# Kernel optimization log

Measured on AMD Instinct MI355X. Metric: run time of the kernel, lower is better.

Reference implementation:

```python
import jax, jax.numpy as jnp
import numpy as np

B, T, N, P = 4, 512, 160, 32
DT2_DX2 = 0.16  # (dt/dx)^2, chosen CFL-stable for c in [1, 1.5]


def setup_inputs() -> dict:
    key = jax.random.key(0)
    k1, k2, k3, k4, k5 = jax.random.split(key, 5)
    x = 0.1 * jax.random.normal(k1, (B, T), dtype=jnp.float32)          # source waveform per batch
    c = 1.0 + 0.5 * jax.random.uniform(k2, (N, N), dtype=jnp.float32)   # wave speed field
    rho = 1.0 + 0.5 * jax.random.uniform(k3, (N, N), dtype=jnp.float32) # density field
    probe_i = jax.random.randint(k4, (P,), 0, N)
    probe_j = jax.random.randint(k5, (P,), 0, N)
    return {
        "x": x, "c": c, "rho": rho,
        "src_i": 80, "src_j": 80,
        "probe_i": probe_i, "probe_j": probe_j,
    }


def _laplacian(h):
    # 5-point stencil with zero-Dirichlet boundaries; h: [B, N, N]
    hp = jnp.pad(h, ((0, 0), (1, 1), (1, 1)))
    return (hp[:, 2:, 1:-1] + hp[:, :-2, 1:-1]
            + hp[:, 1:-1, 2:] + hp[:, 1:-1, :-2] - 4.0 * h)


def reference(x, c, rho, src_i, src_j, probe_i, probe_j):
    coeff = (DT2_DX2 * c * c / rho).astype(x.dtype)  # [N, N]

    def step(carry, xi):
        h1, h2 = carry
        hn = 2.0 * h1 - h2 + coeff * _laplacian(h1)   # leapfrog cell update
        hn = hn.at[:, src_i, src_j].add(xi)           # source injection, xi: [B]
        y = hn[:, probe_i, probe_j]                   # probe readout -> [B, P]
        return (hn, h1), y

    h0 = jnp.zeros((x.shape[0], c.shape[0], c.shape[1]), dtype=x.dtype)
    (_, _), ys = jax.lax.scan(step, (h0, h0), x.T)    # ys: [T, B, P]
    return jnp.transpose(ys, (1, 0, 2))               # [B, T, P]
```

## Files before the change

kernel.cpp:

```cpp
#include <hip/hip_runtime.h>


#define NB   4
#define NBK  4
#define OWN  40
#define D_EX 20
#define NT   512
#define NN   160
#define NP   32
#define C_DT 0.16f

#define TGX   32
#define TPR   16
#define NTHR  (TPR*TGX)
#define EROWS (2*TPR + 2)
#define K_ENT 6

#define SLAB      (D_EX*NN)
#define GB_FLOATS (NB*NBK*2*2*SLAB)
#define FLAG_OFF  (GB_FLOATS*4)

typedef float f4 __attribute__((ext_vector_type(4)));

#if defined(__has_builtin)
#if __has_builtin(__builtin_amdgcn_update_dpp)
#define HAVE_DPP 1
#endif
#endif

__device__ __forceinline__ float shr1(float v) {
#ifdef HAVE_DPP
    return __int_as_float(__builtin_amdgcn_update_dpp(
        0, __float_as_int(v), 0x138 , 0xf, 0xf, true));
#else
    return __shfl_up(v, 1, 64);
#endif
}
__device__ __forceinline__ float shl1(float v) {
#ifdef HAVE_DPP
    return __int_as_float(__builtin_amdgcn_update_dpp(
        0, __float_as_int(v), 0x130 , 0xf, 0xf, true));
#else
    return __shfl_down(v, 1, 64);
#endif
}

__global__ __launch_bounds__(NTHR, 1) void wave_kernel(
    const float* __restrict__ x,
    const float* __restrict__ cmat,
    const float* __restrict__ rho,
    const int*   __restrict__ src_i_p,
    const int*   __restrict__ src_j_p,
    const int*   __restrict__ probe_i,
    const int*   __restrict__ probe_j,
    float*       __restrict__ y,
    float*       __restrict__ gw,
    int*         __restrict__ flags)
{
    __shared__ f4    eb4[2][EROWS][TGX];
    __shared__ float eb1[2][EROWS][TGX];
    __shared__ float xbuf[NT];
    __shared__ int   pco[2*NP];

    const int bid   = blockIdx.x;
    const int batch = bid & 7;
    if (batch >= NB) return;
    const int blk   = bid >> 3;

    const int own_s = blk * OWN;
    const int own_e = own_s + OWN;
    const int ext_s = (own_s - D_EX < 0)  ? 0  : own_s - D_EX;
    const int ext_e = (own_e + D_EX > NN) ? NN : own_e + D_EX;
    const int npr   = (ext_e - ext_s) / 5;

    const int tid = threadIdx.x;
    const int pr  = tid >> 5;
    const int cg  = tid & 31;
    const bool act = pr < npr;
    const int gr0 = ext_s + 5*pr;
    const int c0  = 5*cg;

    {
        float* e4 = (float*)&eb4[0][0][0];
        for (int i = tid; i < 2*EROWS*TGX*4; i += NTHR) e4[i] = 0.0f;
        float* e1 = &eb1[0][0][0];
        for (int i = tid; i < 2*EROWS*TGX; i += NTHR) e1[i] = 0.0f;
        for (int i = tid; i < NT; i += NTHR) xbuf[i] = x[batch*NT + i];
        if (tid < NP) { pco[tid] = probe_i[tid]; pco[NP + tid] = probe_j[tid]; }
    }

    const int si = src_i_p[0];
    const int sj = src_j_p[0];

    float hA[5][5], hB[5][5], cf[5][5], c2[5][5];
    #pragma unroll
    for (int i = 0; i < 5; ++i)
        #pragma unroll
        for (int j = 0; j < 5; ++j) {
            float cfv = 0.0f;
            if (act) {
                const float cc = cmat[(gr0+i)*NN + (c0+j)];
                const float rr = rho[(gr0+i)*NN + (c0+j)];
                cfv = C_DT * cc * cc / rr;
            }
            cf[i][j] = cfv;
            c2[i][j] = 2.0f - 4.0f * cfv;
            hA[i][j] = 0.0f;
            hB[i][j] = 0.0f;
        }

    unsigned srcMask = 0;
    if (act && gr0 <= si && si < gr0 + 5 && c0 <= sj && sj < c0 + 5)
        srcMask = 1u << ((si - gr0)*5 + (sj - c0));

    __syncthreads();

    unsigned long long ent = 0;
    int ecnt = 0;
    if (act && gr0 >= own_s && gr0 < own_e) {
        for (int p = 0; p < NP; ++p) {
            const int r = pco[p], c = pco[NP + p];
            if (r >= gr0 && r < gr0 + 5 && c >= c0 && c < c0 + 5) {
                const int ij = (r - gr0)*5 + (c - c0);
                if (ecnt < K_ENT)
                    ent |= ((unsigned long long)(unsigned)(p | (ij << 5))) << (10*ecnt);
                ecnt++;
            }
        }
    }

    const int bid2 = batch*NBK + blk;
    float* sTop = nullptr; float* sBot = nullptr;
    const float* rTop = nullptr; const float* rBot = nullptr;
    if (blk > 0 && gr0 >= own_s && gr0 < own_s + D_EX)
        sTop = gw + (size_t)(bid2*2 + 0)*2*SLAB + (gr0 - own_s)*NN + c0;
    if (blk < NBK-1 && gr0 >= own_e - D_EX && gr0 < own_e)
        sBot = gw + (size_t)(bid2*2 + 1)*2*SLAB + (gr0 - (own_e - D_EX))*NN + c0;
    if (blk > 0 && act && gr0 < own_s)
        rTop = gw + (size_t)((bid2-1)*2 + 1)*2*SLAB + (gr0 - (own_s - D_EX))*NN + c0;
    if (blk < NBK-1 && act && gr0 >= own_e)
        rBot = gw + (size_t)((bid2+1)*2 + 0)*2*SLAB + (gr0 - own_e)*NN + c0;
    int* const flagSelf = &flags[bid2];
    int* const flagUp   = &flags[bid2 - 1];
    int* const flagDn   = &flags[bid2 + 1];

    float* const yb = y + (size_t)batch*NT*NP;

#define STEP(HS, HD, TT, PIN, POUT)                                           \
    {                                                                         \
        const int tt = (TT);                                                  \
        const f4    nh4 = eb4[PIN][2*pr    ][cg];                             \
        const float nhe = eb1[PIN][2*pr    ][cg];                             \
        const f4    sh4 = eb4[PIN][2*pr + 3][cg];                             \
        const float she = eb1[PIN][2*pr + 3][cg];                             \
        const float nh[5] = { nh4[0], nh4[1], nh4[2], nh4[3], nhe };          \
        const float sh[5] = { sh4[0], sh4[1], sh4[2], sh4[3], she };          \
        float wh[5], eh[5];                                                   \
        _Pragma("unroll")                                                     \
        for (int i = 0; i < 5; ++i) {                                         \
            const float tw = shr1(HS[i][4]);                                  \
            wh[i] = (cg == 0) ? 0.0f : tw;                                    \
            const float te = shl1(HS[i][0]);                                  \
            eh[i] = (cg == TGX-1) ? 0.0f : te;                                \
        }                                                                     \
        _Pragma("unroll")                                                     \
        for (int i = 0; i < 5; ++i) {                                         \
            _Pragma("unroll")                                                 \
            for (int j = 0; j < 5; ++j) {                                     \
                const float up = (i == 0) ? nh[j] : HS[i-1][j];               \
                const float dn = (i == 4) ? sh[j] : HS[i+1][j];               \
                const float lf = (j == 0) ? wh[i] : HS[i][j-1];               \
                const float rt = (j == 4) ? eh[i] : HS[i][j+1];               \
                const float s  = (up + dn) + (lf + rt);                       \
                const float t1 = __builtin_fmaf(c2[i][j], HS[i][j], -HD[i][j]); \
                HD[i][j] = __builtin_fmaf(cf[i][j], s, t1);                   \
            }                                                                 \
        }                                                                     \
        if (srcMask) {                                                        \
            const float xt = xbuf[tt];                                        \
            _Pragma("unroll")                                                 \
            for (int i = 0; i < 5; ++i)                                       \
                _Pragma("unroll")                                             \
                for (int j = 0; j < 5; ++j)                                   \
                    if (srcMask & (1u << (i*5 + j))) HD[i][j] += xt;          \
        }                                                                     \
        eb4[POUT][2*pr + 1][cg] = (f4){ HD[0][0], HD[0][1], HD[0][2], HD[0][3] }; \
        eb1[POUT][2*pr + 1][cg] = HD[0][4];                                   \
        eb4[POUT][2*pr + 2][cg] = (f4){ HD[4][0], HD[4][1], HD[4][2], HD[4][3] }; \
        eb1[POUT][2*pr + 2][cg] = HD[4][4];                                   \
        if (ecnt) {                                                           \
            float* const yt = yb + (size_t)tt * NP;                           \
            _Pragma("unroll")                                                 \
            for (int k = 0; k < K_ENT; ++k) {                                 \
                if (k < ecnt) {                                               \
                    const int e  = (int)((ent >> (10*k)) & 0x3FF);            \
                    const int p  = e & 31;                                    \
                    const int ij = e >> 5;                                    \
                    float v = 0.0f;                                           \
                    _Pragma("unroll")                                         \
                    for (int i = 0; i < 5; ++i)                               \
                        _Pragma("unroll")                                     \
                        for (int j = 0; j < 5; ++j)                           \
                            if (ij == i*5 + j) v = HD[i][j];                  \
                    yt[p] = v;                                                \
                }                                                             \
            }                                                                 \
        }                                                                     \
        __syncthreads();                                                      \
    }

    int t = 0, g = 0;
    while (t < NT) {
        const int steps = (NT - t < D_EX) ? (NT - t) : D_EX;
        for (int k = 0; k < steps; k += 2) {
            STEP(hA, hB, t + k,     0, 1);
            STEP(hB, hA, t + k + 1, 1, 0);
        }
        t += steps;
        if (t >= NT) break;

        if (sTop) {
            #pragma unroll
            for (int i = 0; i < 5; ++i) {
                *(f4*)(sTop + i*NN) = (f4){ hA[i][0], hA[i][1], hA[i][2], hA[i][3] };
                sTop[i*NN + 4] = hA[i][4];
                *(f4*)(sTop + SLAB + i*NN) = (f4){ hB[i][0], hB[i][1], hB[i][2], hB[i][3] };
                sTop[SLAB + i*NN + 4] = hB[i][4];
            }
        }
        if (sBot) {
            #pragma unroll
            for (int i = 0; i < 5; ++i) {
                *(f4*)(sBot + i*NN) = (f4){ hA[i][0], hA[i][1], hA[i][2], hA[i][3] };
                sBot[i*NN + 4] = hA[i][4];
                *(f4*)(sBot + SLAB + i*NN) = (f4){ hB[i][0], hB[i][1], hB[i][2], hB[i][3] };
                sBot[SLAB + i*NN + 4] = hB[i][4];
            }
        }
        __threadfence();
        __syncthreads();
        if (tid == 0) {
            __hip_atomic_fetch_add(flagSelf, 1, __ATOMIC_RELEASE, __HIP_MEMORY_SCOPE_AGENT);
            if (blk > 0)
                while (__hip_atomic_load(flagUp, __ATOMIC_ACQUIRE, __HIP_MEMORY_SCOPE_AGENT) < g + 1) {}
            if (blk < NBK-1)
                while (__hip_atomic_load(flagDn, __ATOMIC_ACQUIRE, __HIP_MEMORY_SCOPE_AGENT) < g + 1) {}
        }
        __syncthreads();
        {
            const float* rp = rTop ? rTop : rBot;
            if (rp) {
                #pragma unroll
                for (int i = 0; i < 5; ++i) {
                    const f4 v1 = *(const f4*)(rp + i*NN);
                    hA[i][0] = v1[0]; hA[i][1] = v1[1]; hA[i][2] = v1[2]; hA[i][3] = v1[3];
                    hA[i][4] = rp[i*NN + 4];
                    const f4 v2 = *(const f4*)(rp + SLAB + i*NN);
                    hB[i][0] = v2[0]; hB[i][1] = v2[1]; hB[i][2] = v2[2]; hB[i][3] = v2[3];
                    hB[i][4] = rp[SLAB + i*NN + 4];
                }
                eb4[0][2*pr + 1][cg] = (f4){ hA[0][0], hA[0][1], hA[0][2], hA[0][3] };
                eb1[0][2*pr + 1][cg] = hA[0][4];
                eb4[0][2*pr + 2][cg] = (f4){ hA[4][0], hA[4][1], hA[4][2], hA[4][3] };
                eb1[0][2*pr + 2][cg] = hA[4][4];
            }
        }
        __syncthreads();
        g++;
    }
#undef STEP
}

extern "C" void kernel_launch(void* const* d_in, const int* in_sizes, int n_in,
                              void* d_out, int out_size, void* d_ws, size_t ws_size,
                              hipStream_t stream) {
    const float* x    = (const float*)d_in[0];
    const float* cmat = (const float*)d_in[1];
    const float* rho  = (const float*)d_in[2];
    const int*   si   = (const int*)d_in[3];
    const int*   sj   = (const int*)d_in[4];
    const int*   pi   = (const int*)d_in[5];
    const int*   pj   = (const int*)d_in[6];
    float*       yout = (float*)d_out;
    float*       gbuf = (float*)d_ws;
    int*         flg  = (int*)((char*)d_ws + FLAG_OFF);

    hipMemsetAsync(flg, 0, NB*NBK*sizeof(int), stream);

    wave_kernel<<<NB*8, NTHR, 0, stream>>>(x, cmat, rho, si, sj, pi, pj,
                                           yout, gbuf, flg);
}
```

Baseline: 644.6 us.

## Exchange intra-wave halo rows via cross-half shuffles, halve LDS halo traffic

Pairs of 32-thread row groups that share a 64-lane wavefront now exchange their adjacent boundary rows with a cross-half shuffle instead of going through LDS. Only the halo rows crossing wavefront boundaries are written to and read from shared memory, which roughly halves the per-step LDS stores and loads and shrinks the halo buffer. The cost is extra shuffle instructions and select logic that depends on row parity, plus more complex edge handling.

Result: slower. 692.6 us (+7.4%).

```diff
diff --git a/kernel.cpp b/kernel.cpp
--- a/kernel.cpp
+++ b/kernel.cpp
@@ -10,11 +10,11 @@
 #define NP   32
 #define C_DT 0.16f
 
-#define TGX   32
-#define TPR   16
-#define NTHR  (TPR*TGX)
-#define EROWS (2*TPR + 2)
-#define K_ENT 6
+#define TGX    32
+#define TPR    16
+#define NTHR   (TPR*TGX)
+#define ESLOTS (TPR + 2)
+#define K_ENT  6
 
 #define SLAB      (D_EX*NN)
 #define GB_FLOATS (NB*NBK*2*2*SLAB)
@@ -57,8 +57,8 @@
     float*       __restrict__ gw,
     int*         __restrict__ flags)
 {
-    __shared__ f4    eb4[2][EROWS][TGX];
-    __shared__ float eb1[2][EROWS][TGX];
+    __shared__ f4    eb4[2][ESLOTS][TGX];
+    __shared__ float eb1[2][ESLOTS][TGX];
     __shared__ float xbuf[NT];
     __shared__ int   pco[2*NP];
 
@@ -76,15 +76,16 @@
     const int tid = threadIdx.x;
     const int pr  = tid >> 5;
     const int cg  = tid & 31;
+    const int oddr = pr & 1;
     const bool act = pr < npr;
     const int gr0 = ext_s + 5*pr;
     const int c0  = 5*cg;
 
     {
         float* e4 = (float*)&eb4[0][0][0];
-        for (int i = tid; i < 2*EROWS*TGX*4; i += NTHR) e4[i] = 0.0f;
+        for (int i = tid; i < 2*ESLOTS*TGX*4; i += NTHR) e4[i] = 0.0f;
         float* e1 = &eb1[0][0][0];
-        for (int i = tid; i < 2*EROWS*TGX; i += NTHR) e1[i] = 0.0f;
+        for (int i = tid; i < 2*ESLOTS*TGX; i += NTHR) e1[i] = 0.0f;
         for (int i = tid; i < NT; i += NTHR) xbuf[i] = x[batch*NT + i];
         if (tid < NP) { pco[tid] = probe_i[tid]; pco[NP + tid] = probe_j[tid]; }
     }
@@ -146,15 +147,27 @@
 
     float* const yb = y + (size_t)batch*NT*NP;
 
+    const int rdSlot = oddr ? (pr + 2) : pr;
+    const int wrSlot = pr + 1;
+    f4*    const rd4a = &eb4[0][rdSlot][cg]; f4*    const rd4b = &eb4[1][rdSlot][cg];
+    float* const rd1a = &eb1[0][rdSlot][cg]; float* const rd1b = &eb1[1][rdSlot][cg];
+    f4*    const wr4a = &eb4[0][wrSlot][cg]; f4*    const wr4b = &eb4[1][wrSlot][cg];
+    float* const wr1a = &eb1[0][wrSlot][cg]; float* const wr1b = &eb1[1][wrSlot][cg];
+
 #define STEP(HS, HD, TT, PIN, POUT)                                           \
     {                                                                         \
         const int tt = (TT);                                                  \
-        const f4    nh4 = eb4[PIN][2*pr    ][cg];                             \
-        const float nhe = eb1[PIN][2*pr    ][cg];                             \
-        const f4    sh4 = eb4[PIN][2*pr + 3][cg];                             \
-        const float she = eb1[PIN][2*pr + 3][cg];                             \
-        const float nh[5] = { nh4[0], nh4[1], nh4[2], nh4[3], nhe };          \
-        const float sh[5] = { sh4[0], sh4[1], sh4[2], sh4[3], she };          \
+          \
+        const f4    l4 = *(PIN ? rd4b : rd4a);                                \
+        const float l1 = *(PIN ? rd1b : rd1a);                                \
+            \
+        float rcv[5];                                                         \
+        _Pragma("unroll")                                                     \
+        for (int j = 0; j < 5; ++j) {                                         \
+            const float snd = oddr ? HS[0][j] : HS[4][j];                     \
+            rcv[j] = __shfl_xor(snd, 32, 64);                                 \
+        }                                                                     \
+                                                    \
         float wh[5], eh[5];                                                   \
         _Pragma("unroll")                                                     \
         for (int i = 0; i < 5; ++i) {                                         \
@@ -163,17 +176,37 @@
             const float te = shl1(HS[i][0]);                                  \
             eh[i] = (cg == TGX-1) ? 0.0f : te;                                \
         }                                                                     \
+           \
         _Pragma("unroll")                                                     \
-        for (int i = 0; i < 5; ++i) {                                         \
+        for (int i = 1; i < 4; ++i) {                                         \
             _Pragma("unroll")                                                 \
             for (int j = 0; j < 5; ++j) {                                     \
-                const float up = (i == 0) ? nh[j] : HS[i-1][j];               \
-                const float dn = (i == 4) ? sh[j] : HS[i+1][j];               \
                 const float lf = (j == 0) ? wh[i] : HS[i][j-1];               \
                 const float rt = (j == 4) ? eh[i] : HS[i][j+1];               \
-                const float s  = (up + dn) + (lf + rt);                       \
+                const float s  = (HS[i-1][j] + HS[i+1][j]) + (lf + rt);       \
                 const float t1 = __builtin_fmaf(c2[i][j], HS[i][j], -HD[i][j]); \
                 HD[i][j] = __builtin_fmaf(cf[i][j], s, t1);                   \
+            }                                                                 \
+        }                                                                     \
+                                   \
+        _Pragma("unroll")                                                     \
+        for (int j = 0; j < 5; ++j) {                                         \
+            const float lv = (j==0)?l4[0]:(j==1)?l4[1]:(j==2)?l4[2]:(j==3)?l4[3]:l1; \
+            const float nh = oddr ? rcv[j] : lv;                              \
+            const float sh = oddr ? lv : rcv[j];                              \
+            {                                                                 \
+                const float lf = (j == 0) ? wh[0] : HS[0][j-1];               \
+                const float rt = (j == 4) ? eh[0] : HS[0][j+1];               \
+                const float s  = (nh + HS[1][j]) + (lf + rt);                 \
+                const float t1 = __builtin_fmaf(c2[0][j], HS[0][j], -HD[0][j]); \
+                HD[0][j] = __builtin_fmaf(cf[0][j], s, t1);                   \
+            }                                                                 \
+            {                                                                 \
+                const float lf = (j == 0) ? wh[4] : HS[4][j-1];               \
+                const float rt = (j == 4) ? eh[4] : HS[4][j+1];               \
+                const float s  = (HS[3][j] + sh) + (lf + rt);                 \
+                const float t1 = __builtin_fmaf(c2[4][j], HS[4][j], -HD[4][j]); \
+                HD[4][j] = __builtin_fmaf(cf[4][j], s, t1);                   \
             }                                                                 \
         }                                                                     \
         if (srcMask) {                                                        \
@@ -184,16 +217,21 @@
                 for (int j = 0; j < 5; ++j)                                   \
                     if (srcMask & (1u << (i*5 + j))) HD[i][j] += xt;          \
         }                                                                     \
-        eb4[POUT][2*pr + 1][cg] = (f4){ HD[0][0], HD[0][1], HD[0][2], HD[0][3] }; \
-        eb1[POUT][2*pr + 1][cg] = HD[0][4];                                   \
-        eb4[POUT][2*pr + 2][cg] = (f4){ HD[4][0], HD[4][1], HD[4][2], HD[4][3] }; \
-        eb1[POUT][2*pr + 2][cg] = HD[4][4];                                   \
+            \
+        {                                                                     \
+            const f4 ev = (f4){ oddr ? HD[4][0] : HD[0][0],                   \
+                                oddr ? HD[4][1] : HD[0][1],                   \
+                                oddr ? HD[4][2] : HD[0][2],                   \
+                                oddr ? HD[4][3] : HD[0][3] };                 \
+            *(POUT ? wr4b : wr4a) = ev;                                       \
+            *(POUT ? wr1b : wr1a) = oddr ? HD[4][4] : HD[0][4];               \
+        }                                                                     \
         if (ecnt) {                                                           \
             float* const yt = yb + (size_t)tt * NP;                           \
             _Pragma("unroll")                                                 \
-            for (int k = 0; k < K_ENT; ++k) {                                 \
-                if (k < ecnt) {                                               \
-                    const int e  = (int)((ent >> (10*k)) & 0x3FF);            \
+            for (int k2 = 0; k2 < K_ENT; ++k2) {                              \
+                if (k2 < ecnt) {                                              \
+                    const int e  = (int)((ent >> (10*k2)) & 0x3FF);           \
                     const int p  = e & 31;                                    \
                     const int ij = e >> 5;                                    \
                     float v = 0.0f;                                           \
@@ -259,10 +297,12 @@
                     hB[i][0] = v2[0]; hB[i][1] = v2[1]; hB[i][2] = v2[2]; hB[i][3] = v2[3];
                     hB[i][4] = rp[SLAB + i*NN + 4];
                 }
-                eb4[0][2*pr + 1][cg] = (f4){ hA[0][0], hA[0][1], hA[0][2], hA[0][3] };
-                eb1[0][2*pr + 1][cg] = hA[0][4];
-                eb4[0][2*pr + 2][cg] = (f4){ hA[4][0], hA[4][1], hA[4][2], hA[4][3] };
-                eb1[0][2*pr + 2][cg] = hA[4][4];
+                const f4 rv = (f4){ oddr ? hA[4][0] : hA[0][0],
+                                    oddr ? hA[4][1] : hA[0][1],
+                                    oddr ? hA[4][2] : hA[0][2],
+                                    oddr ? hA[4][3] : hA[0][3] };
+                *wr4a = rv;
+                *wr1a = oddr ? hA[4][4] : hA[0][4];
             }
         }
         __syncthreads();
```

## Fuse two leapfrog steps per barrier using a two-deep halo with redundant compute

Applied to the files above, without the earlier changes.

Each thread now advances two time steps per round. It computes an intermediate 7x7 field over its 5x5 tile plus a one-cell halo, using two-row halos exchanged through a reorganised shared-memory buffer. This halves the number of block-wide barriers and LDS exchanges per time step. In exchange it adds redundant stencil work on halo cells, needs more registers for the extended coefficient array and window, and uses a larger shared-memory footprint.

Measured after the change: 915.9 us. +42.1%, slower.

```diff
diff --git a/kernel.cpp b/kernel.cpp
--- a/kernel.cpp
+++ b/kernel.cpp
@@ -13,7 +13,7 @@
 #define TGX   32
 #define TPR   16
 #define NTHR  (TPR*TGX)
-#define EROWS (2*TPR + 2)
+#define NSLOT (TPR + 2)
 #define K_ENT 6
 
 #define SLAB      (D_EX*NN)
@@ -45,6 +45,18 @@
 #endif
 }
 
+#define BROW9(dst, v0,v1,v2,v3,v4) {                                          \
+    dst[2]=(v0); dst[3]=(v1); dst[4]=(v2); dst[5]=(v3); dst[6]=(v4);          \
+    const float _m2 = shr1((v3)), _m1 = shr1((v4));                           \
+    const float _p5 = shl1((v0)), _p6 = shl1((v1));                           \
+    dst[0]=(cg==0)?0.0f:_m2;      dst[1]=(cg==0)?0.0f:_m1;                    \
+    dst[7]=(cg==TGX-1)?0.0f:_p5;  dst[8]=(cg==TGX-1)?0.0f:_p6; }
+
+#define BROW7(dst, v0,v1,v2,v3,v4) {                                          \
+    dst[1]=(v0); dst[2]=(v1); dst[3]=(v2); dst[4]=(v3); dst[5]=(v4);          \
+    const float _m1 = shr1((v4)); const float _p5 = shl1((v0));               \
+    dst[0]=(cg==0)?0.0f:_m1;      dst[6]=(cg==TGX-1)?0.0f:_p5; }
+
 __global__ __launch_bounds__(NTHR, 1) void wave_kernel(
     const float* __restrict__ x,
     const float* __restrict__ cmat,
@@ -57,8 +69,8 @@
     float*       __restrict__ gw,
     int*         __restrict__ flags)
 {
-    __shared__ f4    eb4[2][EROWS][TGX];
-    __shared__ float eb1[2][EROWS][TGX];
+    __shared__ f4    L4[2][6][NSLOT][TGX];
+    __shared__ float L1[2][6][NSLOT][TGX];
     __shared__ float xbuf[NT];
     __shared__ int   pco[2*NP];
 
@@ -81,10 +93,10 @@
     const int c0  = 5*cg;
 
     {
-        float* e4 = (float*)&eb4[0][0][0];
-        for (int i = tid; i < 2*EROWS*TGX*4; i += NTHR) e4[i] = 0.0f;
-        float* e1 = &eb1[0][0][0];
-        for (int i = tid; i < 2*EROWS*TGX; i += NTHR) e1[i] = 0.0f;
+        float* z4 = (float*)&L4[0][0][0][0];
+        for (int i = tid; i < 2*6*NSLOT*TGX*4; i += NTHR) z4[i] = 0.0f;
+        float* z1 = &L1[0][0][0][0];
+        for (int i = tid; i < 2*6*NSLOT*TGX; i += NTHR) z1[i] = 0.0f;
         for (int i = tid; i < NT; i += NTHR) xbuf[i] = x[batch*NT + i];
         if (tid < NP) { pco[tid] = probe_i[tid]; pco[NP + tid] = probe_j[tid]; }
     }
@@ -92,26 +104,35 @@
     const int si = src_i_p[0];
     const int sj = src_j_p[0];
 
-    float hA[5][5], hB[5][5], cf[5][5], c2[5][5];
+    float hA[5][5], hB[5][5], cfx[7][7];
+    #pragma unroll
+    for (int ii = -1; ii <= 5; ++ii)
+        #pragma unroll
+        for (int jj = -1; jj <= 5; ++jj) {
+            float cfv = 0.0f;
+            const int r = gr0 + ii, c = c0 + jj;
+            if (act && r >= 0 && r < NN && c >= 0 && c < NN) {
+                const float cc = cmat[r*NN + c];
+                const float rr = rho[r*NN + c];
+                cfv = C_DT * cc * cc / rr;
+            }
+            cfx[ii+1][jj+1] = cfv;
+        }
     #pragma unroll
     for (int i = 0; i < 5; ++i)
         #pragma unroll
-        for (int j = 0; j < 5; ++j) {
-            float cfv = 0.0f;
-            if (act) {
-                const float cc = cmat[(gr0+i)*NN + (c0+j)];
-                const float rr = rho[(gr0+i)*NN + (c0+j)];
-                cfv = C_DT * cc * cc / rr;
-            }
-            cf[i][j] = cfv;
-            c2[i][j] = 2.0f - 4.0f * cfv;
-            hA[i][j] = 0.0f;
-            hB[i][j] = 0.0f;
-        }
+        for (int j = 0; j < 5; ++j) { hA[i][j] = 0.0f; hB[i][j] = 0.0f; }
 
     unsigned srcMask = 0;
     if (act && gr0 <= si && si < gr0 + 5 && c0 <= sj && sj < c0 + 5)
         srcMask = 1u << ((si - gr0)*5 + (sj - c0));
+    unsigned long long srcW = 0ull;
+    if (act) {
+        for (int ii = -1; ii <= 5; ++ii)
+            for (int jj = -1; jj <= 5; ++jj)
+                if (gr0 + ii == si && c0 + jj == sj)
+                    srcW |= 1ull << ((ii+1)*7 + (jj+1));
+    }
 
     __syncthreads();
 
@@ -146,75 +167,107 @@
 
     float* const yb = y + (size_t)batch*NT*NP;
 
-#define STEP(HS, HD, TT, PIN, POUT)                                           \
-    {                                                                         \
-        const int tt = (TT);                                                  \
-        const f4    nh4 = eb4[PIN][2*pr    ][cg];                             \
-        const float nhe = eb1[PIN][2*pr    ][cg];                             \
-        const f4    sh4 = eb4[PIN][2*pr + 3][cg];                             \
-        const float she = eb1[PIN][2*pr + 3][cg];                             \
-        const float nh[5] = { nh4[0], nh4[1], nh4[2], nh4[3], nhe };          \
-        const float sh[5] = { sh4[0], sh4[1], sh4[2], sh4[3], she };          \
-        float wh[5], eh[5];                                                   \
-        _Pragma("unroll")                                                     \
-        for (int i = 0; i < 5; ++i) {                                         \
-            const float tw = shr1(HS[i][4]);                                  \
-            wh[i] = (cg == 0) ? 0.0f : tw;                                    \
-            const float te = shl1(HS[i][0]);                                  \
-            eh[i] = (cg == TGX-1) ? 0.0f : te;                                \
-        }                                                                     \
-        _Pragma("unroll")                                                     \
-        for (int i = 0; i < 5; ++i) {                                         \
-            _Pragma("unroll")                                                 \
-            for (int j = 0; j < 5; ++j) {                                     \
-                const float up = (i == 0) ? nh[j] : HS[i-1][j];               \
-                const float dn = (i == 4) ? sh[j] : HS[i+1][j];               \
-                const float lf = (j == 0) ? wh[i] : HS[i][j-1];               \
-                const float rt = (j == 4) ? eh[i] : HS[i][j+1];               \
-                const float s  = (up + dn) + (lf + rt);                       \
-                const float t1 = __builtin_fmaf(c2[i][j], HS[i][j], -HD[i][j]); \
-                HD[i][j] = __builtin_fmaf(cf[i][j], s, t1);                   \
-            }                                                                 \
-        }                                                                     \
-        if (srcMask) {                                                        \
-            const float xt = xbuf[tt];                                        \
-            _Pragma("unroll")                                                 \
-            for (int i = 0; i < 5; ++i)                                       \
-                _Pragma("unroll")                                             \
-                for (int j = 0; j < 5; ++j)                                   \
-                    if (srcMask & (1u << (i*5 + j))) HD[i][j] += xt;          \
-        }                                                                     \
-        eb4[POUT][2*pr + 1][cg] = (f4){ HD[0][0], HD[0][1], HD[0][2], HD[0][3] }; \
-        eb1[POUT][2*pr + 1][cg] = HD[0][4];                                   \
-        eb4[POUT][2*pr + 2][cg] = (f4){ HD[4][0], HD[4][1], HD[4][2], HD[4][3] }; \
-        eb1[POUT][2*pr + 2][cg] = HD[4][4];                                   \
-        if (ecnt) {                                                           \
-            float* const yt = yb + (size_t)tt * NP;                           \
-            _Pragma("unroll")                                                 \
-            for (int k = 0; k < K_ENT; ++k) {                                 \
-                if (k < ecnt) {                                               \
-                    const int e  = (int)((ent >> (10*k)) & 0x3FF);            \
-                    const int p  = e & 31;                                    \
-                    const int ij = e >> 5;                                    \
-                    float v = 0.0f;                                           \
-                    _Pragma("unroll")                                         \
-                    for (int i = 0; i < 5; ++i)                               \
-                        _Pragma("unroll")                                     \
-                        for (int j = 0; j < 5; ++j)                           \
-                            if (ij == i*5 + j) v = HD[i][j];                  \
-                    yt[p] = v;                                                \
-                }                                                             \
-            }                                                                 \
-        }                                                                     \
-        __syncthreads();                                                      \
-    }
+#define PUBLISH(P) {                                                           \
+    L4[P][0][pr+1][cg]=(f4){hA[0][0],hA[0][1],hA[0][2],hA[0][3]}; L1[P][0][pr+1][cg]=hA[0][4]; \
+    L4[P][1][pr+1][cg]=(f4){hA[1][0],hA[1][1],hA[1][2],hA[1][3]}; L1[P][1][pr+1][cg]=hA[1][4]; \
+    L4[P][2][pr+1][cg]=(f4){hA[3][0],hA[3][1],hA[3][2],hA[3][3]}; L1[P][2][pr+1][cg]=hA[3][4]; \
+    L4[P][3][pr+1][cg]=(f4){hA[4][0],hA[4][1],hA[4][2],hA[4][3]}; L1[P][3][pr+1][cg]=hA[4][4]; \
+    L4[P][4][pr+1][cg]=(f4){hB[0][0],hB[0][1],hB[0][2],hB[0][3]}; L1[P][4][pr+1][cg]=hB[0][4]; \
+    L4[P][5][pr+1][cg]=(f4){hB[4][0],hB[4][1],hB[4][2],hB[4][3]}; L1[P][5][pr+1][cg]=hB[4][4]; }
+
+#define ROUND(T0, PIN, POUT) {                                                 \
+    const int t0 = (T0);                                                       \
+                             \
+    const f4 a2v = L4[PIN][2][pr][cg];   const float a2s = L1[PIN][2][pr][cg]; \
+    const f4 a1v = L4[PIN][3][pr][cg];   const float a1s = L1[PIN][3][pr][cg]; \
+    const f4 b1v = L4[PIN][5][pr][cg];   const float b1s = L1[PIN][5][pr][cg]; \
+    const f4 a5v = L4[PIN][0][pr+2][cg]; const float a5s = L1[PIN][0][pr+2][cg]; \
+    const f4 a6v = L4[PIN][1][pr+2][cg]; const float a6s = L1[PIN][1][pr+2][cg]; \
+    const f4 b5v = L4[PIN][4][pr+2][cg]; const float b5s = L1[PIN][4][pr+2][cg]; \
+    const float xt0 = xbuf[t0], xt1 = xbuf[t0+1];                              \
+    float Xw[3][9];                    \
+    float W[7][7];            \
+    BROW9(Xw[0], a2v[0],a2v[1],a2v[2],a2v[3],a2s);                             \
+    BROW9(Xw[1], a1v[0],a1v[1],a1v[2],a1v[3],a1s);                             \
+    BROW9(Xw[2], hA[0][0],hA[0][1],hA[0][2],hA[0][3],hA[0][4]);                \
+    _Pragma("unroll")                                                          \
+    for (int wr = -1; wr <= 5; ++wr) {                                         \
+        float Yw[7];                                                           \
+        if (wr == -1)     { BROW7(Yw, b1v[0],b1v[1],b1v[2],b1v[3],b1s); }      \
+        else if (wr == 5) { BROW7(Yw, b5v[0],b5v[1],b5v[2],b5v[3],b5s); }      \
+        else { BROW7(Yw, hB[wr][0],hB[wr][1],hB[wr][2],hB[wr][3],hB[wr][4]); } \
+        const int sm = (wr+1)%3, sc = (wr+2)%3, sp = (wr+3)%3;                 \
+        _Pragma("unroll")                                                      \
+        for (int jj = 0; jj < 7; ++jj) {                                       \
+            const float s  = (Xw[sm][jj+1] + Xw[sp][jj+1])                     \
+                           + (Xw[sc][jj]   + Xw[sc][jj+2]);                    \
+            const float h  = Xw[sc][jj+1];                                     \
+            const float lap= __builtin_fmaf(-4.0f, h, s);                      \
+            const float t1 = __builtin_fmaf(2.0f, h, -Yw[jj]);                 \
+            W[wr+1][jj] = __builtin_fmaf(cfx[wr+1][jj], lap, t1);              \
+        }                                                                      \
+        if (wr <= 4) {               \
+            if (wr+2 <= 4) { BROW9(Xw[sm], hA[wr+2][0],hA[wr+2][1],            \
+                                 hA[wr+2][2],hA[wr+2][3],hA[wr+2][4]); }       \
+            else if (wr+2 == 5) { BROW9(Xw[sm], a5v[0],a5v[1],a5v[2],a5v[3],a5s); } \
+            else                { BROW9(Xw[sm], a6v[0],a6v[1],a6v[2],a6v[3],a6s); } \
+        }                                                                      \
+    }                                                                          \
+    if (srcW) {      \
+        _Pragma("unroll")                                                      \
+        for (int ii = 0; ii < 7; ++ii)                                         \
+            _Pragma("unroll")                                                  \
+            for (int jj = 0; jj < 7; ++jj)                                     \
+                if (srcW & (1ull << (ii*7 + jj))) W[ii][jj] += xt0;            \
+    }                                                                          \
+                   \
+    _Pragma("unroll")                                                          \
+    for (int i = 0; i < 5; ++i)                                                \
+        _Pragma("unroll")                                                      \
+        for (int j = 0; j < 5; ++j) {                                          \
+            const float s  = (W[i][j+1] + W[i+2][j+1]) + (W[i+1][j] + W[i+1][j+2]); \
+            const float h  = W[i+1][j+1];                                      \
+            const float lap= __builtin_fmaf(-4.0f, h, s);                      \
+            const float t1 = __builtin_fmaf(2.0f, h, -hA[i][j]);               \
+            hA[i][j] = __builtin_fmaf(cfx[i+1][j+1], lap, t1);                 \
+            hB[i][j] = h;                                                      \
+        }                                                                      \
+    if (srcMask) {                                \
+        _Pragma("unroll")                                                      \
+        for (int i = 0; i < 5; ++i)                                            \
+            _Pragma("unroll")                                                  \
+            for (int j = 0; j < 5; ++j)                                        \
+                if (srcMask & (1u << (i*5 + j))) hA[i][j] += xt1;              \
+    }                                                                          \
+    if (ecnt) {      \
+        float* const yt0 = yb + (size_t)t0 * NP;                               \
+        float* const yt1 = yb + (size_t)(t0+1) * NP;                           \
+        _Pragma("unroll")                                                      \
+        for (int k2 = 0; k2 < K_ENT; ++k2) {                                   \
+            if (k2 < ecnt) {                                                   \
+                const int e  = (int)((ent >> (10*k2)) & 0x3FF);                \
+                const int p  = e & 31;                                         \
+                const int ij = e >> 5;                                         \
+                float v0 = 0.0f, v1 = 0.0f;                                    \
+                _Pragma("unroll")                                              \
+                for (int i = 0; i < 5; ++i)                                    \
+                    _Pragma("unroll")                                          \
+                    for (int j = 0; j < 5; ++j)                                \
+                        if (ij == i*5 + j) { v0 = hB[i][j]; v1 = hA[i][j]; }   \
+                yt0[p] = v0; yt1[p] = v1;                                      \
+            }                                                                  \
+        }                                                                      \
+    }                                                                          \
+    PUBLISH(POUT);                                                             \
+    __syncthreads();                                                           \
+  }
 
     int t = 0, g = 0;
     while (t < NT) {
         const int steps = (NT - t < D_EX) ? (NT - t) : D_EX;
-        for (int k = 0; k < steps; k += 2) {
-            STEP(hA, hB, t + k,     0, 1);
-            STEP(hB, hA, t + k + 1, 1, 0);
+        for (int k = 0; k < steps; k += 4) {
+            ROUND(t + k,     0, 1);
+            ROUND(t + k + 2, 1, 0);
         }
         t += steps;
         if (t >= NT) break;
@@ -259,16 +312,14 @@
                     hB[i][0] = v2[0]; hB[i][1] = v2[1]; hB[i][2] = v2[2]; hB[i][3] = v2[3];
                     hB[i][4] = rp[SLAB + i*NN + 4];
                 }
-                eb4[0][2*pr + 1][cg] = (f4){ hA[0][0], hA[0][1], hA[0][2], hA[0][3] };
-                eb1[0][2*pr + 1][cg] = hA[0][4];
-                eb4[0][2*pr + 2][cg] = (f4){ hA[4][0], hA[4][1], hA[4][2], hA[4][3] };
-                eb1[0][2*pr + 2][cg] = hA[4][4];
-            }
-        }
+            }
+        }
+        PUBLISH(0);
         __syncthreads();
         g++;
     }
-#undef STEP
+#undef ROUND
+#undef PUBLISH
 }
 
 extern "C" void kernel_launch(void* const* d_in, const int* in_sizes, int n_in,
```
